# Optimization experiments

Measured on AMD Instinct MI355X. Metric: run time of the kernel, lower is better.

Reference implementation:

```python
import jax, jax.numpy as jnp
import numpy as np

DIM = 1024
N_HEADS = 16
HEAD_DIM = DIM // N_HEADS


def setup_inputs() -> dict:
    key = jax.random.key(0)
    k_x, k_wqkv, k_bqkv, k_wp, k_bp = jax.random.split(key, 5)
    s = 1.0 / np.sqrt(DIM)
    return {
        "x": jax.random.normal(k_x, (2, 2048, DIM), dtype=jnp.float32),
        "w_qkv": jax.random.uniform(k_wqkv, (3 * DIM, DIM), minval=-s, maxval=s, dtype=jnp.float32),
        "b_qkv": jax.random.uniform(k_bqkv, (3 * DIM,), minval=-s, maxval=s, dtype=jnp.float32),
        "w_proj": jax.random.uniform(k_wp, (DIM, DIM), minval=-s, maxval=s, dtype=jnp.float32),
        "b_proj": jax.random.uniform(k_bp, (DIM,), minval=-s, maxval=s, dtype=jnp.float32),
    }


def reference(x, w_qkv, b_qkv, w_proj, b_proj):
    B, S, D = x.shape
    H, Hd = N_HEADS, HEAD_DIM
    scale = jnp.asarray(Hd, x.dtype) ** 0.5
    qkv = x @ w_qkv.T + b_qkv                      # [B, S, 3D]
    q, k, v = jnp.split(qkv, 3, axis=-1)
    # [B, S, D] -> [B, H, S, Hd]
    q = q.reshape(B, S, H, Hd).transpose(0, 2, 1, 3)
    k = k.reshape(B, S, H, Hd).transpose(0, 2, 1, 3)
    v = v.reshape(B, S, H, Hd).transpose(0, 2, 1, 3)
    attn = jnp.einsum("bhqd,bhkd->bhqk", q, k) / scale
    attn = jax.nn.softmax(attn, axis=-1)
    out = jnp.einsum("bhqk,bhkd->bhqd", attn, v)   # [B, H, S, Hd]
    out = out.transpose(0, 2, 1, 3).reshape(B, S, D)
    return out @ w_proj.T + b_proj
```

## Files before the change

### kernel.cpp

```cpp
#include <hip/hip_runtime.h>

typedef __bf16 bf16;
typedef __bf16 bf16x4 __attribute__((ext_vector_type(4)));
typedef __bf16 bf16x8 __attribute__((ext_vector_type(8)));
typedef float f32x4 __attribute__((ext_vector_type(4)));
typedef float f32x16 __attribute__((ext_vector_type(16)));

#define DIMD 1024
#define NHEAD 16
#define HDIM 64
#define BATCH 2
#define SEQ 2048
#define MTOT (BATCH*SEQ)

#define EXP2F(x) __builtin_amdgcn_exp2f(x)

#define OFF_XB (0ull)
#define OFF_OB (0ull)
#define OFF_VT (8ull<<20)
#define OFF_WP (8ull<<20)

__device__ __forceinline__ void g2l16(const void* g, void* l) {
  __builtin_amdgcn_global_load_lds(
      (const __attribute__((address_space(1))) void*)g,
      (__attribute__((address_space(3))) void*)l,
      16, 0, 0);
}

__device__ __forceinline__ bf16x8 cvt8(float4 a, float4 b) {
  bf16x8 r = { (bf16)a.x, (bf16)a.y, (bf16)a.z, (bf16)a.w,
               (bf16)b.x, (bf16)b.y, (bf16)b.z, (bf16)b.w };
  return r;
}

__global__ __launch_bounds__(256) void cvt_kernel(const float* __restrict__ in,
                                                  bf16* __restrict__ out, int n4) {
  int i = blockIdx.x * blockDim.x + threadIdx.x;
  if (i < n4) {
    float4 v = ((const float4*)in)[i];
    bf16x4 o = { (bf16)v.x, (bf16)v.y, (bf16)v.z, (bf16)v.w };
    ((bf16x4*)out)[i] = o;
  }
}

__global__ __launch_bounds__(256, 3) void gemm_qkv(
    const bf16* __restrict__ A, const float* __restrict__ W,
    const float* __restrict__ bias,
    bf16* __restrict__ Qb, bf16* __restrict__ Kb, bf16* __restrict__ Vt)
{
  __shared__ bf16 lA[2][128 * 32];
  __shared__ bf16 lB[2][128 * 32];
  const int tid = threadIdx.x;
  const int wave = tid >> 6, lane = tid & 63;
  const int l15 = lane & 15, quad = lane >> 4;
  const int wm = wave >> 1, wn = wave & 1;
  const int tm = blockIdx.y * 128, tn = blockIdx.x * 128;

  f32x4 acc[4][4] = {};

  const int srow = tid >> 2, sch = (tid & 3) * 8;
  const bf16*  ga = &A[(size_t)(tm + srow) * DIMD + sch];
  const float* gb = &W[(size_t)(tn + srow) * DIMD + sch];

  g2l16(ga,                     &lA[0][wave * 512]);
  g2l16(ga + (size_t)64 * DIMD, &lA[0][2048 + wave * 512]);
  float4 bv0 = ((const float4*)gb)[0], bv1 = ((const float4*)gb)[1];
  float4 bv2 = ((const float4*)(gb + (size_t)64 * DIMD))[0],
         bv3 = ((const float4*)(gb + (size_t)64 * DIMD))[1];

  for (int kt = 0; kt < 32; kt++) {
    bf16* sB = lB[kt & 1];
    *(bf16x8*)&sB[srow * 32 + sch]        = cvt8(bv0, bv1);
    *(bf16x8*)&sB[(64 + srow) * 32 + sch] = cvt8(bv2, bv3);
    __syncthreads();

    if (kt < 31) {
      const int kn = (kt + 1) * 32;
      bf16* nA = lA[(kt + 1) & 1];
      g2l16(ga + kn,                     &nA[wave * 512]);
      g2l16(ga + kn + (size_t)64 * DIMD, &nA[2048 + wave * 512]);
      const float* gbn = gb + kn;
      bv0 = ((const float4*)gbn)[0]; bv1 = ((const float4*)gbn)[1];
      bv2 = ((const float4*)(gbn + (size_t)64 * DIMD))[0];
      bv3 = ((const float4*)(gbn + (size_t)64 * DIMD))[1];
    }

    const bf16* sA = lA[kt & 1];
    bf16x8 af[4], bfr[4];
#pragma unroll
    for (int i = 0; i < 4; i++)
      af[i] = *(const bf16x8*)&sA[(wm * 64 + i * 16 + l15) * 32 + quad * 8];
#pragma unroll
    for (int i = 0; i < 4; i++)
      bfr[i] = *(const bf16x8*)&sB[(wn * 64 + i * 16 + l15) * 32 + quad * 8];
#pragma unroll
    for (int i = 0; i < 4; i++)
#pragma unroll
      for (int j = 0; j < 4; j++)
        acc[i][j] = __builtin_amdgcn_mfma_f32_16x16x32_bf16(af[i], bfr[j], acc[i][j], 0, 0, 0);
  }

  const int sel = tn >> 10;
#pragma unroll
  for (int j = 0; j < 4; j++) {
    const int n = tn + wn * 64 + j * 16 + l15;
    const float bv = bias[n];
    const int d = n & 1023, h = d >> 6, hd = d & 63;
#pragma unroll
    for (int i = 0; i < 4; i++) {
      const int mbase = tm + wm * 64 + i * 16 + quad * 4;
      const int b = mbase >> 11, s0 = mbase & 2047;
      const int bh = b * NHEAD + h;
      if (sel == 2) {
        bf16x4 vv = { (bf16)(acc[i][j][0] + bv), (bf16)(acc[i][j][1] + bv),
                      (bf16)(acc[i][j][2] + bv), (bf16)(acc[i][j][3] + bv) };
        *(bf16x4*)&Vt[((size_t)bh * HDIM + hd) * SEQ + s0] = vv;
      } else {
#pragma unroll
        for (int r = 0; r < 4; r++) {
          float v = acc[i][j][r] + bv;
          if (sel == 0)
            Qb[((size_t)bh * SEQ + s0 + r) * HDIM + hd] = (bf16)(v * 0.18033688f);
          else
            Kb[((size_t)bh * SEQ + s0 + r) * HDIM + hd] = (bf16)v;
        }
      }
    }
  }
}

__global__ __launch_bounds__(256, 2) void gemm_proj(
    const bf16* __restrict__ A, const bf16* __restrict__ Bt,
    const float* __restrict__ bias, float* __restrict__ out)
{
  __shared__ bf16 lA[2][64 * 32];
  __shared__ bf16 lB[2][128 * 32];
  const int tid = threadIdx.x;
  const int wave = tid >> 6, lane = tid & 63;
  const int l15 = lane & 15, quad = lane >> 4;
  const int tm = blockIdx.y * 64, tn = blockIdx.x * 128;

  f32x4 acc[4][2] = {};

  const int srow = tid >> 2, sch = (tid & 3) * 8;
  const bf16* ga = &A[(size_t)(tm + srow) * DIMD + sch];
  const bf16* gb = &Bt[(size_t)(tn + srow) * DIMD + sch];

  g2l16(ga,                     &lA[0][wave * 512]);
  g2l16(gb,                     &lB[0][wave * 512]);
  g2l16(gb + (size_t)64 * DIMD, &lB[0][2048 + wave * 512]);

  for (int kt = 0; kt < 32; kt++) {
    __syncthreads();

    if (kt < 31) {
      const int kn = (kt + 1) * 32;
      bf16* nA = lA[(kt + 1) & 1];
      bf16* nB = lB[(kt + 1) & 1];
      g2l16(ga + kn,                     &nA[wave * 512]);
      g2l16(gb + kn,                     &nB[wave * 512]);
      g2l16(gb + kn + (size_t)64 * DIMD, &nB[2048 + wave * 512]);
    }

    const bf16* sA = lA[kt & 1];
    const bf16* sB = lB[kt & 1];
    bf16x8 af[4], bfr[2];
#pragma unroll
    for (int i = 0; i < 4; i++)
      af[i] = *(const bf16x8*)&sA[(i * 16 + l15) * 32 + quad * 8];
#pragma unroll
    for (int j = 0; j < 2; j++)
      bfr[j] = *(const bf16x8*)&sB[(wave * 32 + j * 16 + l15) * 32 + quad * 8];
#pragma unroll
    for (int i = 0; i < 4; i++)
#pragma unroll
      for (int j = 0; j < 2; j++)
        acc[i][j] = __builtin_amdgcn_mfma_f32_16x16x32_bf16(af[i], bfr[j], acc[i][j], 0, 0, 0);
  }

#pragma unroll
  for (int j = 0; j < 2; j++) {
    const int n = tn + wave * 32 + j * 16 + l15;
    const float bv = bias[n];
#pragma unroll
    for (int i = 0; i < 4; i++) {
      const int mbase = tm + i * 16 + quad * 4;
#pragma unroll
      for (int r = 0; r < 4; r++)
        out[(size_t)(mbase + r) * DIMD + n] = acc[i][j][r] + bv;
    }
  }
}

#define KTILE 128
#define KSTR 72
#define VSTR 136
__global__ __launch_bounds__(256, 2) void attn_kernel(
    const bf16* __restrict__ Qb, const bf16* __restrict__ Kb,
    const bf16* __restrict__ Vt, bf16* __restrict__ Ob)
{
  __shared__ bf16 lK[KTILE * KSTR];
  __shared__ bf16 lV[64 * VSTR];

  const int tid = threadIdx.x;
  const int wave = tid >> 6, lane = tid & 63;
  const int l31 = lane & 31, h = lane >> 5;
  const int xcd = blockIdx.x & 7, grp = blockIdx.x >> 3;
  const int bh = xcd + 8 * (grp & 3);
  const int qt = grp >> 2;

  const int qrow = qt * 128 + wave * 32 + l31;
  const bf16* qp = Qb + ((size_t)bh * SEQ + qrow) * HDIM + h * 8;
  bf16x8 qf[4];
#pragma unroll
  for (int c = 0; c < 4; c++) qf[c] = *(const bf16x8*)(qp + c * 16);

  const int srow = tid >> 3;
  const int sch = (tid & 7) * 8;
  const bf16* kg = Kb + ((size_t)bh * SEQ + srow) * HDIM + sch;
  const bf16* vg = Vt + ((size_t)bh * HDIM + srow) * SEQ + sch;

  uint4 kr[4], vr[4];
#pragma unroll
  for (int i = 0; i < 4; i++)
    kr[i] = *(const uint4*)(kg + (size_t)(32 * i) * HDIM);
#pragma unroll
  for (int i = 0; i < 2; i++)
#pragma unroll
    for (int j = 0; j < 2; j++)
      vr[i * 2 + j] = *(const uint4*)(vg + (size_t)(32 * i) * SEQ + j * 64);

#pragma unroll
  for (int i = 0; i < 4; i++)
    *(uint4*)&lK[(srow + 32 * i) * KSTR + sch] = kr[i];
#pragma unroll
  for (int i = 0; i < 2; i++)
#pragma unroll
    for (int j = 0; j < 2; j++)
      *(uint4*)&lV[(srow + 32 * i) * VSTR + j * 64 + sch] = vr[i * 2 + j];

  f32x16 o0 = {}, o1 = {};
  float mrow = -1e30f, lrow = 0.f;

  for (int kt = 0; kt < SEQ / KTILE; kt++) {
    __syncthreads();

    if (kt < SEQ / KTILE - 1) {
      const size_t koff = (size_t)(kt + 1) * KTILE;
#pragma unroll
      for (int i = 0; i < 4; i++)
        kr[i] = *(const uint4*)(kg + (koff + 32 * i) * HDIM);
#pragma unroll
      for (int i = 0; i < 2; i++)
#pragma unroll
        for (int j = 0; j < 2; j++)
          vr[i * 2 + j] = *(const uint4*)(vg + (size_t)(32 * i) * SEQ + koff + j * 64);
    }

    f32x16 s0 = {}, s1 = {}, s2 = {}, s3 = {};
#pragma unroll
    for (int c = 0; c < 4; c++) {
      bf16x8 k0 = *(const bf16x8*)&lK[(l31)       * KSTR + c * 16 + h * 8];
      bf16x8 k1 = *(const bf16x8*)&lK[(32 + l31)  * KSTR + c * 16 + h * 8];
      bf16x8 k2 = *(const bf16x8*)&lK[(64 + l31)  * KSTR + c * 16 + h * 8];
      bf16x8 k3 = *(const bf16x8*)&lK[(96 + l31)  * KSTR + c * 16 + h * 8];
      s0 = __builtin_amdgcn_mfma_f32_32x32x16_bf16(k0, qf[c], s0, 0, 0, 0);
      s1 = __builtin_amdgcn_mfma_f32_32x32x16_bf16(k1, qf[c], s1, 0, 0, 0);
      s2 = __builtin_amdgcn_mfma_f32_32x32x16_bf16(k2, qf[c], s2, 0, 0, 0);
      s3 = __builtin_amdgcn_mfma_f32_32x32x16_bf16(k3, qf[c], s3, 0, 0, 0);
    }

    float a[16];
#pragma unroll
    for (int r = 0; r < 16; r++)
      a[r] = fmaxf(fmaxf(s0[r], s1[r]), fmaxf(s2[r], s3[r]));
#pragma unroll
    for (int r = 0; r < 8; r++) a[r] = fmaxf(a[r], a[r + 8]);
#pragma unroll
    for (int r = 0; r < 4; r++) a[r] = fmaxf(a[r], a[r + 4]);
    float mx = fmaxf(fmaxf(a[0], a[1]), fmaxf(a[2], a[3]));
    mx = fmaxf(mx, __shfl_xor(mx, 32, 64));

    const float nm = fmaxf(mrow, mx);
    const float alpha = EXP2F(mrow - nm);
    mrow = nm;

#pragma unroll
    for (int r = 0; r < 16; r++) {
      s0[r] = EXP2F(s0[r] - nm);
      s1[r] = EXP2F(s1[r] - nm);
      s2[r] = EXP2F(s2[r] - nm);
      s3[r] = EXP2F(s3[r] - nm);
    }
#pragma unroll
    for (int r = 0; r < 16; r++)
      a[r] = (s0[r] + s1[r]) + (s2[r] + s3[r]);
#pragma unroll
    for (int r = 0; r < 8; r++) a[r] += a[r + 8];
#pragma unroll
    for (int r = 0; r < 4; r++) a[r] += a[r + 4];
    float rs = (a[0] + a[1]) + (a[2] + a[3]);
    rs += __shfl_xor(rs, 32, 64);
    lrow = lrow * alpha + rs;

#pragma unroll
    for (int r = 0; r < 16; r++) { o0[r] *= alpha; o1[r] *= alpha; }

#pragma unroll
    for (int g = 0; g < 4; g++) {
      const f32x16& sg = (g == 0) ? s0 : (g == 1) ? s1 : (g == 2) ? s2 : s3;
#pragma unroll
      for (int cp = 0; cp < 2; cp++) {
        bf16x4 pk0 = { (bf16)sg[8 * cp + 0], (bf16)sg[8 * cp + 1],
                       (bf16)sg[8 * cp + 2], (bf16)sg[8 * cp + 3] };
        bf16x4 pk1 = { (bf16)sg[8 * cp + 4], (bf16)sg[8 * cp + 5],
                       (bf16)sg[8 * cp + 6], (bf16)sg[8 * cp + 7] };
        uint2 w0 = *(uint2*)&pk0;
        uint2 w1 = *(uint2*)&pk1;
        unsigned send0 = h ? w0.x : w1.x;
        unsigned send1 = h ? w0.y : w1.y;
        unsigned recv0 = __shfl_xor(send0, 32, 64);
        unsigned recv1 = __shfl_xor(send1, 32, 64);
        union { unsigned u[4]; bf16x8 v; } f;
        f.u[0] = h ? recv0 : w0.x;
        f.u[1] = h ? recv1 : w0.y;
        f.u[2] = h ? w1.x : recv0;
        f.u[3] = h ? w1.y : recv1;
        const int cc = 2 * g + cp;
        bf16x8 v0 = *(const bf16x8*)&lV[(l31)      * VSTR + cc * 16 + h * 8];
        bf16x8 v1 = *(const bf16x8*)&lV[(32 + l31) * VSTR + cc * 16 + h * 8];
        o0 = __builtin_amdgcn_mfma_f32_32x32x16_bf16(v0, f.v, o0, 0, 0, 0);
        o1 = __builtin_amdgcn_mfma_f32_32x32x16_bf16(v1, f.v, o1, 0, 0, 0);
      }
    }

    __syncthreads();

    if (kt < SEQ / KTILE - 1) {
#pragma unroll
      for (int i = 0; i < 4; i++)
        *(uint4*)&lK[(srow + 32 * i) * KSTR + sch] = kr[i];
#pragma unroll
      for (int i = 0; i < 2; i++)
#pragma unroll
        for (int j = 0; j < 2; j++)
          *(uint4*)&lV[(srow + 32 * i) * VSTR + j * 64 + sch] = vr[i * 2 + j];
    }
  }

  const int b = bh >> 4, head = bh & 15;
  const float inv = 1.f / lrow;
  const size_t base = ((size_t)b * SEQ + qrow) * DIMD + head * HDIM;
#pragma unroll
  for (int g = 0; g < 4; g++) {
    bf16x4 oa = { (bf16)(o0[4*g] * inv), (bf16)(o0[4*g+1] * inv),
                  (bf16)(o0[4*g+2] * inv), (bf16)(o0[4*g+3] * inv) };
    bf16x4 ob = { (bf16)(o1[4*g] * inv), (bf16)(o1[4*g+1] * inv),
                  (bf16)(o1[4*g+2] * inv), (bf16)(o1[4*g+3] * inv) };
    *(bf16x4*)&Ob[base + g * 8 + h * 4]      = oa;
    *(bf16x4*)&Ob[base + 32 + g * 8 + h * 4] = ob;
  }
}

extern "C" void kernel_launch(void* const* d_in, const int* in_sizes, int n_in,
                              void* d_out, int out_size, void* d_ws, size_t ws_size,
                              hipStream_t stream) {
  const float* x      = (const float*)d_in[0];
  const float* w_qkv  = (const float*)d_in[1];
  const float* b_qkv  = (const float*)d_in[2];
  const float* w_proj = (const float*)d_in[3];
  const float* b_proj = (const float*)d_in[4];
  float* out = (float*)d_out;
  char* ws = (char*)d_ws;

  bf16* Qb = (bf16*)d_out;
  bf16* Kb = (bf16*)d_out + (size_t)MTOT * DIMD;
  bf16* xb     = (bf16*)(ws + OFF_XB);
  bf16* Ob     = (bf16*)(ws + OFF_OB);
  bf16* Vt     = (bf16*)(ws + OFF_VT);
  bf16* wprojb = (bf16*)(ws + OFF_WP);

  cvt_kernel<<<(MTOT * DIMD / 4) / 256, 256, 0, stream>>>(x, xb, MTOT * DIMD / 4);
  gemm_qkv<<<dim3(24, 32), 256, 0, stream>>>(xb, w_qkv, b_qkv, Qb, Kb, Vt);
  attn_kernel<<<BATCH * NHEAD * (SEQ / 128), 256, 0, stream>>>(Qb, Kb, Vt, Ob);
  cvt_kernel<<<(DIMD * DIMD / 4) / 256, 256, 0, stream>>>(w_proj, wprojb, DIMD * DIMD / 4);
  gemm_proj<<<dim3(8, 64), 256, 0, stream>>>(Ob, wprojb, b_proj, out);
}
```

Before: 231.7 us.

## Double-buffer attention LDS, split softmax into two halves, remap QKV GEMM tiles per XCD

The attention kernel now double-buffers the K/V LDS tiles and writes each prefetched tile at the top of the iteration. It also splits the 128-key tile into two 64-key halves, each with its own online-softmax update and PV MFMAs, so exp work can interleave with matrix work. The QKV GEMM grid is remapped so each XCD handles a contiguous group of N tiles, aiming for better L2 reuse of the weights. The cost is doubled LDS per block, which may reduce occupancy, plus an extra alpha rescale of the output accumulators each iteration. The second __syncthreads is kept even though double buffering could allow dropping it.

```diff
diff --git a/kernel.cpp b/kernel.cpp
--- a/kernel.cpp
+++ b/kernel.cpp
@@ -54,7 +54,12 @@
   const int wave = tid >> 6, lane = tid & 63;
   const int l15 = lane & 15, quad = lane >> 4;
   const int wm = wave >> 1, wn = wave & 1;
-  const int tm = blockIdx.y * 128, tn = blockIdx.x * 128;
+
+  const int lin = blockIdx.y * 24 + blockIdx.x;
+  const int xcd = lin & 7, idx = lin >> 3;
+  const int tn_i = xcd * 3 + idx % 3;
+  const int tm_i = idx / 3;
+  const int tm = tm_i * 128, tn = tn_i * 128;
 
   f32x4 acc[4][4] = {};
 
@@ -192,15 +197,14 @@
   }
 }
 
-#define KTILE 128
 #define KSTR 72
 #define VSTR 136
 __global__ __launch_bounds__(256, 2) void attn_kernel(
     const bf16* __restrict__ Qb, const bf16* __restrict__ Kb,
     const bf16* __restrict__ Vt, bf16* __restrict__ Ob)
 {
-  __shared__ bf16 lK[KTILE * KSTR];
-  __shared__ bf16 lV[64 * VSTR];
+  __shared__ bf16 lK[2][128 * KSTR];
+  __shared__ bf16 lV[2][64 * VSTR];
 
   const int tid = threadIdx.x;
   const int wave = tid >> 6, lane = tid & 63;
@@ -228,25 +232,26 @@
   for (int i = 0; i < 2; i++)
 #pragma unroll
     for (int j = 0; j < 2; j++)
-      vr[i * 2 + j] = *(const uint4*)(vg + (size_t)(32 * i) * SEQ + j * 64);
-
-#pragma unroll
-  for (int i = 0; i < 4; i++)
-    *(uint4*)&lK[(srow + 32 * i) * KSTR + sch] = kr[i];
-#pragma unroll
-  for (int i = 0; i < 2; i++)
-#pragma unroll
-    for (int j = 0; j < 2; j++)
-      *(uint4*)&lV[(srow + 32 * i) * VSTR + j * 64 + sch] = vr[i * 2 + j];
+      vr[2 * i + j] = *(const uint4*)(vg + (size_t)(32 * i) * SEQ + j * 64);
 
   f32x16 o0 = {}, o1 = {};
   float mrow = -1e30f, lrow = 0.f;
 
-  for (int kt = 0; kt < SEQ / KTILE; kt++) {
+  for (int kt = 0; kt < SEQ / 128; kt++) {
+    bf16* sK = lK[kt & 1];
+    bf16* sV = lV[kt & 1];
+#pragma unroll
+    for (int i = 0; i < 4; i++)
+      *(uint4*)&sK[(srow + 32 * i) * KSTR + sch] = kr[i];
+#pragma unroll
+    for (int i = 0; i < 2; i++)
+#pragma unroll
+      for (int j = 0; j < 2; j++)
+        *(uint4*)&sV[(srow + 32 * i) * VSTR + j * 64 + sch] = vr[2 * i + j];
     __syncthreads();
 
-    if (kt < SEQ / KTILE - 1) {
-      const size_t koff = (size_t)(kt + 1) * KTILE;
+    if (kt < SEQ / 128 - 1) {
+      const size_t koff = (size_t)(kt + 1) * 128;
 #pragma unroll
       for (int i = 0; i < 4; i++)
         kr[i] = *(const uint4*)(kg + (koff + 32 * i) * HDIM);
@@ -254,98 +259,134 @@
       for (int i = 0; i < 2; i++)
 #pragma unroll
         for (int j = 0; j < 2; j++)
-          vr[i * 2 + j] = *(const uint4*)(vg + (size_t)(32 * i) * SEQ + koff + j * 64);
+          vr[2 * i + j] = *(const uint4*)(vg + (size_t)(32 * i) * SEQ + koff + j * 64);
     }
 
     f32x16 s0 = {}, s1 = {}, s2 = {}, s3 = {};
 #pragma unroll
     for (int c = 0; c < 4; c++) {
-      bf16x8 k0 = *(const bf16x8*)&lK[(l31)       * KSTR + c * 16 + h * 8];
-      bf16x8 k1 = *(const bf16x8*)&lK[(32 + l31)  * KSTR + c * 16 + h * 8];
-      bf16x8 k2 = *(const bf16x8*)&lK[(64 + l31)  * KSTR + c * 16 + h * 8];
-      bf16x8 k3 = *(const bf16x8*)&lK[(96 + l31)  * KSTR + c * 16 + h * 8];
+      bf16x8 k0 = *(const bf16x8*)&sK[(l31)      * KSTR + c * 16 + h * 8];
+      bf16x8 k1 = *(const bf16x8*)&sK[(32 + l31) * KSTR + c * 16 + h * 8];
       s0 = __builtin_amdgcn_mfma_f32_32x32x16_bf16(k0, qf[c], s0, 0, 0, 0);
       s1 = __builtin_amdgcn_mfma_f32_32x32x16_bf16(k1, qf[c], s1, 0, 0, 0);
+    }
+#pragma unroll
+    for (int c = 0; c < 4; c++) {
+      bf16x8 k2 = *(const bf16x8*)&sK[(64 + l31) * KSTR + c * 16 + h * 8];
+      bf16x8 k3 = *(const bf16x8*)&sK[(96 + l31) * KSTR + c * 16 + h * 8];
       s2 = __builtin_amdgcn_mfma_f32_32x32x16_bf16(k2, qf[c], s2, 0, 0, 0);
       s3 = __builtin_amdgcn_mfma_f32_32x32x16_bf16(k3, qf[c], s3, 0, 0, 0);
     }
 
-    float a[16];
-#pragma unroll
-    for (int r = 0; r < 16; r++)
-      a[r] = fmaxf(fmaxf(s0[r], s1[r]), fmaxf(s2[r], s3[r]));
-#pragma unroll
-    for (int r = 0; r < 8; r++) a[r] = fmaxf(a[r], a[r + 8]);
-#pragma unroll
-    for (int r = 0; r < 4; r++) a[r] = fmaxf(a[r], a[r + 4]);
-    float mx = fmaxf(fmaxf(a[0], a[1]), fmaxf(a[2], a[3]));
-    mx = fmaxf(mx, __shfl_xor(mx, 32, 64));
-
-    const float nm = fmaxf(mrow, mx);
-    const float alpha = EXP2F(mrow - nm);
-    mrow = nm;
-
-#pragma unroll
-    for (int r = 0; r < 16; r++) {
-      s0[r] = EXP2F(s0[r] - nm);
-      s1[r] = EXP2F(s1[r] - nm);
-      s2[r] = EXP2F(s2[r] - nm);
-      s3[r] = EXP2F(s3[r] - nm);
-    }
-#pragma unroll
-    for (int r = 0; r < 16; r++)
-      a[r] = (s0[r] + s1[r]) + (s2[r] + s3[r]);
-#pragma unroll
-    for (int r = 0; r < 8; r++) a[r] += a[r + 8];
-#pragma unroll
-    for (int r = 0; r < 4; r++) a[r] += a[r + 4];
-    float rs = (a[0] + a[1]) + (a[2] + a[3]);
-    rs += __shfl_xor(rs, 32, 64);
-    lrow = lrow * alpha + rs;
-
-#pragma unroll
-    for (int r = 0; r < 16; r++) { o0[r] *= alpha; o1[r] *= alpha; }
-
-#pragma unroll
-    for (int g = 0; g < 4; g++) {
-      const f32x16& sg = (g == 0) ? s0 : (g == 1) ? s1 : (g == 2) ? s2 : s3;
-#pragma unroll
-      for (int cp = 0; cp < 2; cp++) {
-        bf16x4 pk0 = { (bf16)sg[8 * cp + 0], (bf16)sg[8 * cp + 1],
-                       (bf16)sg[8 * cp + 2], (bf16)sg[8 * cp + 3] };
-        bf16x4 pk1 = { (bf16)sg[8 * cp + 4], (bf16)sg[8 * cp + 5],
-                       (bf16)sg[8 * cp + 6], (bf16)sg[8 * cp + 7] };
-        uint2 w0 = *(uint2*)&pk0;
-        uint2 w1 = *(uint2*)&pk1;
-        unsigned send0 = h ? w0.x : w1.x;
-        unsigned send1 = h ? w0.y : w1.y;
-        unsigned recv0 = __shfl_xor(send0, 32, 64);
-        unsigned recv1 = __shfl_xor(send1, 32, 64);
-        union { unsigned u[4]; bf16x8 v; } f;
-        f.u[0] = h ? recv0 : w0.x;
-        f.u[1] = h ? recv1 : w0.y;
-        f.u[2] = h ? w1.x : recv0;
-        f.u[3] = h ? w1.y : recv1;
-        const int cc = 2 * g + cp;
-        bf16x8 v0 = *(const bf16x8*)&lV[(l31)      * VSTR + cc * 16 + h * 8];
-        bf16x8 v1 = *(const bf16x8*)&lV[(32 + l31) * VSTR + cc * 16 + h * 8];
-        o0 = __builtin_amdgcn_mfma_f32_32x32x16_bf16(v0, f.v, o0, 0, 0, 0);
-        o1 = __builtin_amdgcn_mfma_f32_32x32x16_bf16(v1, f.v, o1, 0, 0, 0);
+    {
+      float mx = -1e30f;
+#pragma unroll
+      for (int r = 0; r < 16; r++) { mx = fmaxf(mx, s0[r]); mx = fmaxf(mx, s1[r]); }
+      mx = fmaxf(mx, __shfl_xor(mx, 32, 64));
+      const float nm = fmaxf(mrow, mx);
+      const float alpha = EXP2F(mrow - nm);
+      mrow = nm;
+      float rs = 0.f;
+#pragma unroll
+      for (int r = 0; r < 16; r++) {
+        const float p0 = EXP2F(s0[r] - nm);
+        const float p1 = EXP2F(s1[r] - nm);
+        s0[r] = p0; s1[r] = p1;
+        rs += p0 + p1;
+      }
+      rs += __shfl_xor(rs, 32, 64);
+      lrow = lrow * alpha + rs;
+#pragma unroll
+      for (int r = 0; r < 16; r++) { o0[r] *= alpha; o1[r] *= alpha; }
+
+      bf16x8 pfA[4];
+#pragma unroll
+      for (int g = 0; g < 2; g++) {
+        const f32x16& sg = (g == 0) ? s0 : s1;
+#pragma unroll
+        for (int cp = 0; cp < 2; cp++) {
+          bf16x4 pk0 = { (bf16)sg[8 * cp + 0], (bf16)sg[8 * cp + 1],
+                         (bf16)sg[8 * cp + 2], (bf16)sg[8 * cp + 3] };
+          bf16x4 pk1 = { (bf16)sg[8 * cp + 4], (bf16)sg[8 * cp + 5],
+                         (bf16)sg[8 * cp + 6], (bf16)sg[8 * cp + 7] };
+          uint2 w0 = *(uint2*)&pk0;
+          uint2 w1 = *(uint2*)&pk1;
+          unsigned send0 = h ? w0.x : w1.x;
+          unsigned send1 = h ? w0.y : w1.y;
+          unsigned recv0 = __shfl_xor(send0, 32, 64);
+          unsigned recv1 = __shfl_xor(send1, 32, 64);
+          union { unsigned u[4]; bf16x8 v; } f;
+          f.u[0] = h ? recv0 : w0.x;
+          f.u[1] = h ? recv1 : w0.y;
+          f.u[2] = h ? w1.x : recv0;
+          f.u[3] = h ? w1.y : recv1;
+          pfA[2 * g + cp] = f.v;
+        }
+      }
+#pragma unroll
+      for (int c = 0; c < 4; c++) {
+        bf16x8 v0 = *(const bf16x8*)&sV[(l31)      * VSTR + c * 16 + h * 8];
+        bf16x8 v1 = *(const bf16x8*)&sV[(32 + l31) * VSTR + c * 16 + h * 8];
+        o0 = __builtin_amdgcn_mfma_f32_32x32x16_bf16(v0, pfA[c], o0, 0, 0, 0);
+        o1 = __builtin_amdgcn_mfma_f32_32x32x16_bf16(v1, pfA[c], o1, 0, 0, 0);
+      }
+    }
+
+    {
+      float mx = -1e30f;
+#pragma unroll
+      for (int r = 0; r < 16; r++) { mx = fmaxf(mx, s2[r]); mx = fmaxf(mx, s3[r]); }
+      mx = fmaxf(mx, __shfl_xor(mx, 32, 64));
+      const float nm = fmaxf(mrow, mx);
+      const float alpha = EXP2F(mrow - nm);
+      mrow = nm;
+      float rs = 0.f;
+#pragma unroll
+      for (int r = 0; r < 16; r++) {
+        const float p0 = EXP2F(s2[r] - nm);
+        const float p1 = EXP2F(s3[r] - nm);
+        s2[r] = p0; s3[r] = p1;
+        rs += p0 + p1;
+      }
+      rs += __shfl_xor(rs, 32, 64);
+      lrow = lrow * alpha + rs;
+#pragma unroll
+      for (int r = 0; r < 16; r++) { o0[r] *= alpha; o1[r] *= alpha; }
+
+      bf16x8 pfB[4];
+#pragma unroll
+      for (int g = 0; g < 2; g++) {
+        const f32x16& sg = (g == 0) ? s2 : s3;
+#pragma unroll
+        for (int cp = 0; cp < 2; cp++) {
+          bf16x4 pk0 = { (bf16)sg[8 * cp + 0], (bf16)sg[8 * cp + 1],
+                         (bf16)sg[8 * cp + 2], (bf16)sg[8 * cp + 3] };
+          bf16x4 pk1 = { (bf16)sg[8 * cp + 4], (bf16)sg[8 * cp + 5],
+                         (bf16)sg[8 * cp + 6], (bf16)sg[8 * cp + 7] };
+          uint2 w0 = *(uint2*)&pk0;
+          uint2 w1 = *(uint2*)&pk1;
+          unsigned send0 = h ? w0.x : w1.x;
+          unsigned send1 = h ? w0.y : w1.y;
+          unsigned recv0 = __shfl_xor(send0, 32, 64);
+          unsigned recv1 = __shfl_xor(send1, 32, 64);
+          union { unsigned u[4]; bf16x8 v; } f;
+          f.u[0] = h ? recv0 : w0.x;
+          f.u[1] = h ? recv1 : w0.y;
+          f.u[2] = h ? w1.x : recv0;
+          f.u[3] = h ? w1.y : recv1;
+          pfB[2 * g + cp] = f.v;
+        }
+      }
+#pragma unroll
+      for (int c = 0; c < 4; c++) {
+        bf16x8 v0 = *(const bf16x8*)&sV[(l31)      * VSTR + 64 + c * 16 + h * 8];
+        bf16x8 v1 = *(const bf16x8*)&sV[(32 + l31) * VSTR + 64 + c * 16 + h * 8];
+        o0 = __builtin_amdgcn_mfma_f32_32x32x16_bf16(v0, pfB[c], o0, 0, 0, 0);
+        o1 = __builtin_amdgcn_mfma_f32_32x32x16_bf16(v1, pfB[c], o1, 0, 0, 0);
       }
     }
 
     __syncthreads();
-
-    if (kt < SEQ / KTILE - 1) {
-#pragma unroll
-      for (int i = 0; i < 4; i++)
-        *(uint4*)&lK[(srow + 32 * i) * KSTR + sch] = kr[i];
-#pragma unroll
-      for (int i = 0; i < 2; i++)
-#pragma unroll
-        for (int j = 0; j < 2; j++)
-          *(uint4*)&lV[(srow + 32 * i) * VSTR + j * 64 + sch] = vr[i * 2 + j];
-    }
   }
 
   const int b = bh >> 4, head = bh & 15;
```

New measurement: 239.7 us. 3.4% more time.
